# Kernel optimization log

Hardware: AMD Instinct MI355X
Metric: run time of the kernel (lower is better)

The kernel has to match this reference:

```python
import jax, jax.numpy as jnp
import numpy as np
from jax import lax

FILTERS = 256
KERNEL = 1
BATCH, T, D = 16, 2048, 512


def conv1d_same(x, w, b):
    # x: [B, T, Cin], w: [K, Cin, Cout], b: [Cout]
    y = lax.conv_general_dilated(
        x, w, window_strides=(1,), padding='SAME',
        dimension_numbers=('NWC', 'WIO', 'NWC'))
    return y + b


def setup_inputs() -> dict:
    key = jax.random.key(0)
    ks = jax.random.split(key, 5)
    inputs = jax.random.normal(ks[0], (BATCH, T, D), dtype=jnp.float32)
    # Glorot-ish init for conv kernels
    W_qkv = jax.random.normal(ks[1], (KERNEL, D, 3 * FILTERS), dtype=jnp.float32) * (1.0 / np.sqrt(D))
    b_qkv = jnp.zeros((3 * FILTERS,), dtype=jnp.float32)
    W_out = jax.random.normal(ks[2], (KERNEL, FILTERS, D), dtype=jnp.float32) * (1.0 / np.sqrt(FILTERS))
    b_out = jnp.zeros((D,), dtype=jnp.float32)
    return {"inputs": inputs, "W_qkv": W_qkv, "b_qkv": b_qkv, "W_out": W_out, "b_out": b_out}


def reference(inputs, W_qkv, b_qkv, W_out, b_out):
    # QKV projection: conv1d(kernel=1) == pointwise linear, kept general via conv
    qkv = conv1d_same(inputs, W_qkv, b_qkv)          # [B, T, 3F]
    q, k, v = jnp.split(qkv, 3, axis=-1)             # each [B, T, F]
    scale = jnp.sqrt(jnp.asarray(FILTERS, dtype=q.dtype))
    score = jnp.einsum('btf,bsf->bts', q, k) / scale  # [B, T, T]
    attn = jax.nn.softmax(score, axis=-1)
    context = jnp.einsum('bts,bsf->btf', attn, v)    # [B, T, F]
    output = conv1d_same(context, W_out, b_out)      # [B, T, D]
    return inputs + output
```

## Files before the change

### kernel.cpp

```cpp
#include <hip/hip_runtime.h>

typedef __bf16 bf16_t;
typedef __attribute__((ext_vector_type(8))) __bf16 bf16x8;
typedef __attribute__((ext_vector_type(4))) __bf16 bf16x4;
typedef __attribute__((ext_vector_type(4))) float f32x4;

#define GLL16(gsrc, ldst)                                                                   \
  __builtin_amdgcn_global_load_lds(                                                         \
      (const __attribute__((address_space(1))) unsigned int*)(gsrc),                        \
      (__attribute__((address_space(3))) unsigned int*)(ldst), 16, 0, 0)

#define BATCH 16
#define TT    2048
#define DD    512
#define FF    256
#define MTOT  (BATCH * TT)

__global__ __launch_bounds__(256) void cast_all_kernel(const float* __restrict__ x,
                                                       bf16_t* __restrict__ xb,
                                                       const float* __restrict__ Wqkv,
                                                       const float* __restrict__ Wout,
                                                       bf16_t* __restrict__ WqkvT,
                                                       bf16_t* __restrict__ WoutT) {
  const int t0 = blockIdx.x * blockDim.x + threadIdx.x;
  const int stride = gridDim.x * blockDim.x;
  const int n4 = (MTOT * DD) / 4;
  for (int i = t0; i < n4; i += stride) {
    float4 v = ((const float4*)x)[i];
    bf16x4 o;
    o[0] = (bf16_t)v.x; o[1] = (bf16_t)v.y; o[2] = (bf16_t)v.z; o[3] = (bf16_t)v.w;
    ((bf16x4*)xb)[i] = o;
  }
  for (int i = t0; i < 768 * 512 + 512 * 256; i += stride) {
    if (i < 768 * 512) {
      int n = i >> 9, k = i & 511;
      WqkvT[i] = (bf16_t)Wqkv[k * 768 + n];
    } else {
      int i2 = i - 768 * 512;
      int n = i2 >> 8, k = i2 & 255;
      WoutT[i2] = (bf16_t)Wout[k * 512 + n];
    }
  }
}

__global__ __launch_bounds__(256) void gemm_qkv_kernel(const bf16_t* __restrict__ A,
                                                       const bf16_t* __restrict__ Bt,
                                                       const float* __restrict__ bias,
                                                       bf16_t* __restrict__ Qo,
                                                       bf16_t* __restrict__ Ko,
                                                       bf16_t* __restrict__ Vt) {
  __shared__ __align__(16) bf16_t Al[2][128 * 32];
  __shared__ __align__(16) bf16_t Bl[2][128 * 32];
  const int tid = threadIdx.x;
  const int l = tid & 63, w = tid >> 6;
  const int g = l >> 4, r = l & 15;
  const int wm = w >> 1, wn = w & 1;
  const int lin = blockIdx.x;
  const int wid = (lin & 7) * 192 + (lin >> 3);
  const int m0 = (wid / 6) * 128;
  const int n0 = (wid % 6) * 128;
  const int lda = 512, ldb = 512;
  const bf16_t* Abase = A + (size_t)m0 * lda;
  const bf16_t* Bbase = Bt + (size_t)n0 * ldb;

  f32x4 acc[4][4] = {};

  auto stage = [&](int kt, int bufi) {
    const int k0 = kt * 32;
#pragma unroll
    for (int rnd = 0; rnd < 2; ++rnd) {
      int idx = rnd * 256 + tid;
      int row = idx >> 2, d = idx & 3;
      int sc = d ^ ((row >> 1) & 3);
      GLL16(Abase + row * lda + k0 + sc * 8, &Al[bufi][idx * 8]);
    }
#pragma unroll
    for (int rnd = 0; rnd < 2; ++rnd) {
      int idx = rnd * 256 + tid;
      int row = idx >> 2, d = idx & 3;
      int sc = d ^ ((row >> 1) & 3);
      GLL16(Bbase + row * ldb + k0 + sc * 8, &Bl[bufi][idx * 8]);
    }
  };

  stage(0, 0);
  __syncthreads();
  int buf = 0;
  const int NK = 512 / 32;
  for (int kt = 0; kt < NK; ++kt) {
    if (kt + 1 < NK) stage(kt + 1, buf ^ 1);
    bf16x8 af[4], bfr[4];
#pragma unroll
    for (int mi = 0; mi < 4; ++mi) {
      int row = wm * 64 + mi * 16 + r;
      int cc = g ^ ((row >> 1) & 3);
      af[mi] = *(const bf16x8*)&Al[buf][row * 32 + cc * 8];
    }
#pragma unroll
    for (int ni = 0; ni < 4; ++ni) {
      int row = wn * 64 + ni * 16 + r;
      int cc = g ^ ((row >> 1) & 3);
      bfr[ni] = *(const bf16x8*)&Bl[buf][row * 32 + cc * 8];
    }
#pragma unroll
    for (int mi = 0; mi < 4; ++mi)
#pragma unroll
      for (int ni = 0; ni < 4; ++ni)
        acc[mi][ni] = __builtin_amdgcn_mfma_f32_16x16x32_bf16(af[mi], bfr[ni], acc[mi][ni], 0, 0, 0);
    __syncthreads();
    buf ^= 1;
  }

  const int qsel = n0 >> 8;
#pragma unroll
  for (int mi = 0; mi < 4; ++mi) {
    int row0 = m0 + wm * 64 + mi * 16 + g * 4;
#pragma unroll
    for (int ni = 0; ni < 4; ++ni) {
      int col = n0 + wn * 64 + ni * 16 + r;
      float bv = bias[col];
      int cl = col & 255;
      if (qsel == 2) {
        bf16x4 pk;
#pragma unroll
        for (int i = 0; i < 4; ++i) pk[i] = (bf16_t)(acc[mi][ni][i] + bv);
        int b = row0 >> 11, t0 = row0 & 2047;
        *(bf16x4*)&Vt[((size_t)(b * 256 + cl)) * 2048 + t0] = pk;
      } else {
        bf16_t* dst = (qsel == 0) ? Qo : Ko;
#pragma unroll
        for (int i = 0; i < 4; ++i)
          dst[(size_t)(row0 + i) * 256 + cl] = (bf16_t)(acc[mi][ni][i] + bv);
      }
    }
  }
}

__global__ __launch_bounds__(256, 2) void attn_kernel(const bf16_t* __restrict__ Q,
                                                      const bf16_t* __restrict__ K,
                                                      const bf16_t* __restrict__ Vt,
                                                      bf16_t* __restrict__ ctx) {
  __shared__ __align__(16) bf16_t Kl[2][32 * 256];
  __shared__ __align__(16) bf16_t Vl[2][256 * 32];
  __shared__ __align__(16) bf16_t Pl[4][16 * 32];
  const int tid = threadIdx.x;
  const int l = tid & 63, w = tid >> 6;
  const int g = l >> 4, r = l & 15;
  const int lin = blockIdx.x;
  const int wid = (lin & 7) * 64 + (lin >> 3);
  const int b = wid >> 5;
  const int q0 = (wid & 31) * 64 + w * 16;
  const bf16_t* Kb = K + ((size_t)b * TT) * 256;
  const bf16_t* Vb = Vt + (size_t)b * 256 * TT;

  bf16x8 qf[8];
  const bf16_t* Qrow = Q + ((size_t)(b * TT) + q0 + r) * 256;
#pragma unroll
  for (int kf = 0; kf < 8; ++kf) qf[kf] = *(const bf16x8*)(Qrow + kf * 32 + g * 8);

  f32x4 cacc[16] = {};
  float m_run = -3.0e38f, l_run = 0.0f;

  auto stage = [&](int kv0, int bi) {
#pragma unroll
    for (int rnd = 0; rnd < 4; ++rnd) {
      int idx = rnd * 256 + tid;
      int row = idx >> 5, d = idx & 31;
      int sc = d ^ (row & 7);
      GLL16(Kb + (size_t)(kv0 + row) * 256 + sc * 8, &Kl[bi][idx * 8]);
    }
#pragma unroll
    for (int rnd = 0; rnd < 4; ++rnd) {
      int idx = rnd * 256 + tid;
      int row = idx >> 2, d = idx & 3;
      GLL16(Vb + (size_t)row * TT + kv0 + d * 8, &Vl[bi][idx * 8]);
    }
  };

  stage(0, 0);
  __syncthreads();
  int buf = 0;

  for (int kv0 = 0; kv0 < TT; kv0 += 32) {
    if (kv0 + 32 < TT) stage(kv0 + 32, buf ^ 1);

    f32x4 st[2] = {};
    __builtin_amdgcn_s_setprio(1);
#pragma unroll
    for (int kf = 0; kf < 8; ++kf) {
#pragma unroll
      for (int kvf = 0; kvf < 2; ++kvf) {
        int row = kvf * 16 + r;
        int chunk = (kf * 4 + g) ^ (r & 7);
        bf16x8 kfr = *(const bf16x8*)&Kl[buf][row * 256 + chunk * 8];
        st[kvf] = __builtin_amdgcn_mfma_f32_16x16x32_bf16(kfr, qf[kf], st[kvf], 0, 0, 0);
      }
    }
    __builtin_amdgcn_s_setprio(0);

    float s[2][4];
    float tmax = -3.0e38f;
#pragma unroll
    for (int kvf = 0; kvf < 2; ++kvf)
#pragma unroll
      for (int i = 0; i < 4; ++i) {
        s[kvf][i] = st[kvf][i] * 0.0625f;
        tmax = fmaxf(tmax, s[kvf][i]);
      }
    tmax = fmaxf(tmax, __shfl_xor(tmax, 16));
    tmax = fmaxf(tmax, __shfl_xor(tmax, 32));
    if (!__all(tmax - m_run <= 8.0f)) {
      float mnew = fmaxf(m_run, tmax);
      float alpha = __expf(m_run - mnew);
      l_run *= alpha;
#pragma unroll
      for (int fc = 0; fc < 16; ++fc)
#pragma unroll
        for (int i = 0; i < 4; ++i) cacc[fc][i] *= alpha;
      m_run = mnew;
    }
    float psum = 0.0f;
#pragma unroll
    for (int kvf = 0; kvf < 2; ++kvf) {
      bf16x4 pk;
#pragma unroll
      for (int i = 0; i < 4; ++i) {
        float p = __expf(s[kvf][i] - m_run);
        psum += p;
        pk[i] = (bf16_t)p;
      }
      int eidx = r * 32 + (((kvf * 2 + (g >> 1)) ^ (r & 3)) << 3) + (g & 1) * 4;
      *(bf16x4*)&Pl[w][eidx] = pk;
    }
    psum += __shfl_xor(psum, 16);
    psum += __shfl_xor(psum, 32);
    l_run += psum;

    bf16x8 pf = *(const bf16x8*)&Pl[w][r * 32 + ((g ^ (r & 3)) << 3)];
    __builtin_amdgcn_s_setprio(1);
#pragma unroll
    for (int fc = 0; fc < 16; ++fc) {
      int row = fc * 16 + r;
      bf16x8 vf = *(const bf16x8*)&Vl[buf][row * 32 + g * 8];
      cacc[fc] = __builtin_amdgcn_mfma_f32_16x16x32_bf16(vf, pf, cacc[fc], 0, 0, 0);
    }
    __builtin_amdgcn_s_setprio(0);

    __syncthreads();
    buf ^= 1;
  }

  float inv = 1.0f / l_run;
  bf16_t* crow = ctx + ((size_t)(b * TT) + q0 + r) * 256;
#pragma unroll
  for (int fc = 0; fc < 16; ++fc) {
    bf16x4 pk;
#pragma unroll
    for (int i = 0; i < 4; ++i) pk[i] = (bf16_t)(cacc[fc][i] * inv);
    *(bf16x4*)(crow + fc * 16 + g * 4) = pk;
  }
}

__global__ __launch_bounds__(256) void gemm_out_kernel(const bf16_t* __restrict__ A,
                                                       const bf16_t* __restrict__ Bt,
                                                       const float* __restrict__ bias,
                                                       const float* __restrict__ X,
                                                       float* __restrict__ Out) {
  __shared__ __align__(16) bf16_t Al[2][128 * 32];
  __shared__ __align__(16) bf16_t Bl[2][128 * 32];
  const int tid = threadIdx.x;
  const int l = tid & 63, w = tid >> 6;
  const int g = l >> 4, r = l & 15;
  const int wm = w >> 1, wn = w & 1;
  const int lin = blockIdx.x;
  const int wid = (lin & 7) * 128 + (lin >> 3);
  const int m0 = (wid >> 2) * 128;
  const int n0 = (wid & 3) * 128;
  const int lda = 256, ldb = 256;
  const bf16_t* Abase = A + (size_t)m0 * lda;
  const bf16_t* Bbase = Bt + (size_t)n0 * ldb;

  f32x4 acc[4][4] = {};

  auto stage = [&](int kt, int bufi) {
    const int k0 = kt * 32;
#pragma unroll
    for (int rnd = 0; rnd < 2; ++rnd) {
      int idx = rnd * 256 + tid;
      int row = idx >> 2, d = idx & 3;
      int sc = d ^ ((row >> 1) & 3);
      GLL16(Abase + row * lda + k0 + sc * 8, &Al[bufi][idx * 8]);
    }
#pragma unroll
    for (int rnd = 0; rnd < 2; ++rnd) {
      int idx = rnd * 256 + tid;
      int row = idx >> 2, d = idx & 3;
      int sc = d ^ ((row >> 1) & 3);
      GLL16(Bbase + row * ldb + k0 + sc * 8, &Bl[bufi][idx * 8]);
    }
  };

  stage(0, 0);
  __syncthreads();
  int buf = 0;
  const int NK = 256 / 32;
  for (int kt = 0; kt < NK; ++kt) {
    if (kt + 1 < NK) stage(kt + 1, buf ^ 1);
    bf16x8 af[4], bfr[4];
#pragma unroll
    for (int mi = 0; mi < 4; ++mi) {
      int row = wm * 64 + mi * 16 + r;
      int cc = g ^ ((row >> 1) & 3);
      af[mi] = *(const bf16x8*)&Al[buf][row * 32 + cc * 8];
    }
#pragma unroll
    for (int ni = 0; ni < 4; ++ni) {
      int row = wn * 64 + ni * 16 + r;
      int cc = g ^ ((row >> 1) & 3);
      bfr[ni] = *(const bf16x8*)&Bl[buf][row * 32 + cc * 8];
    }
#pragma unroll
    for (int mi = 0; mi < 4; ++mi)
#pragma unroll
      for (int ni = 0; ni < 4; ++ni)
        acc[mi][ni] = __builtin_amdgcn_mfma_f32_16x16x32_bf16(af[mi], bfr[ni], acc[mi][ni], 0, 0, 0);
    __syncthreads();
    buf ^= 1;
  }

#pragma unroll
  for (int mi = 0; mi < 4; ++mi) {
    int row0 = m0 + wm * 64 + mi * 16 + g * 4;
#pragma unroll
    for (int ni = 0; ni < 4; ++ni) {
      int col = n0 + wn * 64 + ni * 16 + r;
      float bv = bias[col];
#pragma unroll
      for (int i = 0; i < 4; ++i) {
        size_t off = (size_t)(row0 + i) * 512 + col;
        Out[off] = acc[mi][ni][i] + bv + X[off];
      }
    }
  }
}

extern "C" void kernel_launch(void* const* d_in, const int* in_sizes, int n_in,
                              void* d_out, int out_size, void* d_ws, size_t ws_size,
                              hipStream_t stream) {
  const float* X    = (const float*)d_in[0];
  const float* Wqkv = (const float*)d_in[1];
  const float* bqkv = (const float*)d_in[2];
  const float* Wout = (const float*)d_in[3];
  const float* bout = (const float*)d_in[4];
  float* out = (float*)d_out;

  char* ws = (char*)d_ws;
  bf16_t* Xbf   = (bf16_t*)ws;
  bf16_t* ctx   = Xbf;
  bf16_t* WqkvT = (bf16_t*)(ws + 33554432);
  bf16_t* WoutT = (bf16_t*)(ws + 34340864);
  bf16_t* Qb    = (bf16_t*)(ws + 34603008);
  bf16_t* Kb    = (bf16_t*)(ws + 51380224);
  bf16_t* Vt    = (bf16_t*)(ws + 68157440);

  cast_all_kernel<<<2048, 256, 0, stream>>>(X, Xbf, Wqkv, Wout, WqkvT, WoutT);
  gemm_qkv_kernel<<<1536, 256, 0, stream>>>(Xbf, WqkvT, bqkv, Qb, Kb, Vt);
  attn_kernel<<<512, 256, 0, stream>>>(Qb, Kb, Vt, ctx);
  gemm_out_kernel<<<1024, 256, 0, stream>>>(ctx, WoutT, bout, X, out);
}
```

Baseline: 328.2 us.

## Process two query groups per wave to reuse K/V fragments across MFMAs

The attention kernel now runs 2 waves per block, each handling 32 query rows as two 16-row groups. Every K and V fragment read from LDS feeds two MFMAs, halving LDS traffic per MFMA. The V tile in LDS gets a new XOR-swizzled layout, and each thread issues twice as many async copies because the block is smaller. The cost is higher register pressure (doubled accumulators and Q fragments) and only 128 threads per block, which may lower occupancy and latency hiding.

New measurement: 376.5 us. 1.15x slower.

```diff
diff --git a/kernel.cpp b/kernel.cpp
--- a/kernel.cpp
+++ b/kernel.cpp
@@ -136,44 +136,50 @@
   }
 }
 
-__global__ __launch_bounds__(256, 2) void attn_kernel(const bf16_t* __restrict__ Q,
+__global__ __launch_bounds__(128, 2) void attn_kernel(const bf16_t* __restrict__ Q,
                                                       const bf16_t* __restrict__ K,
                                                       const bf16_t* __restrict__ Vt,
                                                       bf16_t* __restrict__ ctx) {
   __shared__ __align__(16) bf16_t Kl[2][32 * 256];
-  __shared__ __align__(16) bf16_t Vl[2][256 * 32];
-  __shared__ __align__(16) bf16_t Pl[4][16 * 32];
+  __shared__ __align__(16) bf16_t Vl[2][128 * 64];
+  __shared__ __align__(16) bf16_t Pl[2][2][16 * 32];
   const int tid = threadIdx.x;
   const int l = tid & 63, w = tid >> 6;
   const int g = l >> 4, r = l & 15;
   const int lin = blockIdx.x;
   const int wid = (lin & 7) * 64 + (lin >> 3);
   const int b = wid >> 5;
-  const int q0 = (wid & 31) * 64 + w * 16;
+  const int q0 = (wid & 31) * 64 + w * 32;
   const bf16_t* Kb = K + ((size_t)b * TT) * 256;
   const bf16_t* Vb = Vt + (size_t)b * 256 * TT;
 
-  bf16x8 qf[8];
-  const bf16_t* Qrow = Q + ((size_t)(b * TT) + q0 + r) * 256;
-#pragma unroll
-  for (int kf = 0; kf < 8; ++kf) qf[kf] = *(const bf16x8*)(Qrow + kf * 32 + g * 8);
-
-  f32x4 cacc[16] = {};
-  float m_run = -3.0e38f, l_run = 0.0f;
+  bf16x8 qf[2][8];
+#pragma unroll
+  for (int qg = 0; qg < 2; ++qg) {
+    const bf16_t* Qrow = Q + ((size_t)(b * TT) + q0 + qg * 16 + r) * 256;
+#pragma unroll
+    for (int kf = 0; kf < 8; ++kf) qf[qg][kf] = *(const bf16x8*)(Qrow + kf * 32 + g * 8);
+  }
+
+  f32x4 cacc[16][2] = {};
+  float m_run[2] = {-3.0e38f, -3.0e38f};
+  float l_run[2] = {0.0f, 0.0f};
 
   auto stage = [&](int kv0, int bi) {
 #pragma unroll
-    for (int rnd = 0; rnd < 4; ++rnd) {
-      int idx = rnd * 256 + tid;
+    for (int rnd = 0; rnd < 8; ++rnd) {
+      int idx = rnd * 128 + tid;
       int row = idx >> 5, d = idx & 31;
       int sc = d ^ (row & 7);
       GLL16(Kb + (size_t)(kv0 + row) * 256 + sc * 8, &Kl[bi][idx * 8]);
     }
 #pragma unroll
-    for (int rnd = 0; rnd < 4; ++rnd) {
-      int idx = rnd * 256 + tid;
-      int row = idx >> 2, d = idx & 3;
-      GLL16(Vb + (size_t)row * TT + kv0 + d * 8, &Vl[bi][idx * 8]);
+    for (int rnd = 0; rnd < 8; ++rnd) {
+      int idx = rnd * 128 + tid;
+      int R = idx >> 3, cd = idx & 7;
+      int c = cd ^ (R & 7);
+      int f = 2 * R + (c >> 2);
+      GLL16(Vb + (size_t)f * TT + kv0 + (c & 3) * 8, &Vl[bi][idx * 8]);
     }
   };
 
@@ -184,7 +190,7 @@
   for (int kv0 = 0; kv0 < TT; kv0 += 32) {
     if (kv0 + 32 < TT) stage(kv0 + 32, buf ^ 1);
 
-    f32x4 st[2] = {};
+    f32x4 st[2][2] = {};
     __builtin_amdgcn_s_setprio(1);
 #pragma unroll
     for (int kf = 0; kf < 8; ++kf) {
@@ -193,56 +199,64 @@
         int row = kvf * 16 + r;
         int chunk = (kf * 4 + g) ^ (r & 7);
         bf16x8 kfr = *(const bf16x8*)&Kl[buf][row * 256 + chunk * 8];
-        st[kvf] = __builtin_amdgcn_mfma_f32_16x16x32_bf16(kfr, qf[kf], st[kvf], 0, 0, 0);
+#pragma unroll
+        for (int qg = 0; qg < 2; ++qg)
+          st[kvf][qg] = __builtin_amdgcn_mfma_f32_16x16x32_bf16(kfr, qf[qg][kf], st[kvf][qg], 0, 0, 0);
       }
     }
     __builtin_amdgcn_s_setprio(0);
 
-    float s[2][4];
-    float tmax = -3.0e38f;
-#pragma unroll
-    for (int kvf = 0; kvf < 2; ++kvf)
-#pragma unroll
-      for (int i = 0; i < 4; ++i) {
-        s[kvf][i] = st[kvf][i] * 0.0625f;
-        tmax = fmaxf(tmax, s[kvf][i]);
-      }
-    tmax = fmaxf(tmax, __shfl_xor(tmax, 16));
-    tmax = fmaxf(tmax, __shfl_xor(tmax, 32));
-    if (!__all(tmax - m_run <= 8.0f)) {
-      float mnew = fmaxf(m_run, tmax);
-      float alpha = __expf(m_run - mnew);
-      l_run *= alpha;
-#pragma unroll
-      for (int fc = 0; fc < 16; ++fc)
-#pragma unroll
-        for (int i = 0; i < 4; ++i) cacc[fc][i] *= alpha;
-      m_run = mnew;
-    }
-    float psum = 0.0f;
-#pragma unroll
-    for (int kvf = 0; kvf < 2; ++kvf) {
-      bf16x4 pk;
-#pragma unroll
-      for (int i = 0; i < 4; ++i) {
-        float p = __expf(s[kvf][i] - m_run);
-        psum += p;
-        pk[i] = (bf16_t)p;
-      }
-      int eidx = r * 32 + (((kvf * 2 + (g >> 1)) ^ (r & 3)) << 3) + (g & 1) * 4;
-      *(bf16x4*)&Pl[w][eidx] = pk;
-    }
-    psum += __shfl_xor(psum, 16);
-    psum += __shfl_xor(psum, 32);
-    l_run += psum;
-
-    bf16x8 pf = *(const bf16x8*)&Pl[w][r * 32 + ((g ^ (r & 3)) << 3)];
+#pragma unroll
+    for (int qg = 0; qg < 2; ++qg) {
+      float s[2][4];
+      float tmax = -3.0e38f;
+#pragma unroll
+      for (int kvf = 0; kvf < 2; ++kvf)
+#pragma unroll
+        for (int i = 0; i < 4; ++i) {
+          s[kvf][i] = st[kvf][qg][i] * 0.0625f;
+          tmax = fmaxf(tmax, s[kvf][i]);
+        }
+      tmax = fmaxf(tmax, __shfl_xor(tmax, 16));
+      tmax = fmaxf(tmax, __shfl_xor(tmax, 32));
+      if (!__all(tmax - m_run[qg] <= 8.0f)) {
+        float mnew = fmaxf(m_run[qg], tmax);
+        float alpha = __expf(m_run[qg] - mnew);
+        l_run[qg] *= alpha;
+#pragma unroll
+        for (int fc = 0; fc < 16; ++fc)
+#pragma unroll
+          for (int i = 0; i < 4; ++i) cacc[fc][qg][i] *= alpha;
+        m_run[qg] = mnew;
+      }
+      float psum = 0.0f;
+#pragma unroll
+      for (int kvf = 0; kvf < 2; ++kvf) {
+        bf16x4 pk;
+#pragma unroll
+        for (int i = 0; i < 4; ++i) {
+          float p = __expf(s[kvf][i] - m_run[qg]);
+          psum += p;
+          pk[i] = (bf16_t)p;
+        }
+        int eidx = r * 32 + (((kvf * 2 + (g >> 1)) ^ (r & 3)) << 3) + (g & 1) * 4;
+        *(bf16x4*)&Pl[w][qg][eidx] = pk;
+      }
+      psum += __shfl_xor(psum, 16);
+      psum += __shfl_xor(psum, 32);
+      l_run[qg] += psum;
+    }
+
+    bf16x8 pf0 = *(const bf16x8*)&Pl[w][0][r * 32 + ((g ^ (r & 3)) << 3)];
+    bf16x8 pf1 = *(const bf16x8*)&Pl[w][1][r * 32 + ((g ^ (r & 3)) << 3)];
     __builtin_amdgcn_s_setprio(1);
 #pragma unroll
     for (int fc = 0; fc < 16; ++fc) {
-      int row = fc * 16 + r;
-      bf16x8 vf = *(const bf16x8*)&Vl[buf][row * 32 + g * 8];
-      cacc[fc] = __builtin_amdgcn_mfma_f32_16x16x32_bf16(vf, pf, cacc[fc], 0, 0, 0);
+      int R = fc * 8 + (r >> 1);
+      int cs = ((r & 1) * 4 + g) ^ ((r >> 1) & 7);
+      bf16x8 vfr = *(const bf16x8*)&Vl[buf][R * 64 + cs * 8];
+      cacc[fc][0] = __builtin_amdgcn_mfma_f32_16x16x32_bf16(vfr, pf0, cacc[fc][0], 0, 0, 0);
+      cacc[fc][1] = __builtin_amdgcn_mfma_f32_16x16x32_bf16(vfr, pf1, cacc[fc][1], 0, 0, 0);
     }
     __builtin_amdgcn_s_setprio(0);
 
@@ -250,14 +264,17 @@
     buf ^= 1;
   }
 
-  float inv = 1.0f / l_run;
-  bf16_t* crow = ctx + ((size_t)(b * TT) + q0 + r) * 256;
-#pragma unroll
-  for (int fc = 0; fc < 16; ++fc) {
-    bf16x4 pk;
-#pragma unroll
-    for (int i = 0; i < 4; ++i) pk[i] = (bf16_t)(cacc[fc][i] * inv);
-    *(bf16x4*)(crow + fc * 16 + g * 4) = pk;
+#pragma unroll
+  for (int qg = 0; qg < 2; ++qg) {
+    float inv = 1.0f / l_run[qg];
+    bf16_t* crow = ctx + ((size_t)(b * TT) + q0 + qg * 16 + r) * 256;
+#pragma unroll
+    for (int fc = 0; fc < 16; ++fc) {
+      bf16x4 pk;
+#pragma unroll
+      for (int i = 0; i < 4; ++i) pk[i] = (bf16_t)(cacc[fc][qg][i] * inv);
+      *(bf16x4*)(crow + fc * 16 + g * 4) = pk;
+    }
   }
 }
 
@@ -365,6 +382,6 @@
 
   cast_all_kernel<<<2048, 256, 0, stream>>>(X, Xbf, Wqkv, Wout, WqkvT, WoutT);
   gemm_qkv_kernel<<<1536, 256, 0, stream>>>(Xbf, WqkvT, bqkv, Qb, Kb, Vt);
-  attn_kernel<<<512, 256, 0, stream>>>(Qb, Kb, Vt, ctx);
+  attn_kernel<<<512, 128, 0, stream>>>(Qb, Kb, Vt, ctx);
   gemm_out_kernel<<<1024, 256, 0, stream>>>(ctx, WoutT, bout, X, out);
 }
```

## Split KV in attention, switch to 32x32 MFMA, add merge kernel

Applied to the files above, without the earlier changes.

Attention now splits each batch's KV range into two halves, so each block covers 128 query rows over 1024 keys and writes partial context plus max/sum statistics. A new merge kernel combines the two partials. The inner loops move from 16x16x32 to 32x32x16 MFMA, and P is kept in registers via permlane32 swaps instead of a round trip through LDS, with V swizzled in LDS. The aim is more reuse per K/V tile and less LDS traffic for P. The cost is extra global traffic for the partial contexts and one more kernel launch.

Result: no change. 322.1 us (-1.9%).

```diff
diff --git a/kernel.cpp b/kernel.cpp
--- a/kernel.cpp
+++ b/kernel.cpp
@@ -4,17 +4,27 @@
 typedef __attribute__((ext_vector_type(8))) __bf16 bf16x8;
 typedef __attribute__((ext_vector_type(4))) __bf16 bf16x4;
 typedef __attribute__((ext_vector_type(4))) float f32x4;
+typedef __attribute__((ext_vector_type(16))) float f32x16;
+typedef __attribute__((ext_vector_type(4))) unsigned u32x4;
 
 #define GLL16(gsrc, ldst)                                                                   \
   __builtin_amdgcn_global_load_lds(                                                         \
       (const __attribute__((address_space(1))) unsigned int*)(gsrc),                        \
       (__attribute__((address_space(3))) unsigned int*)(ldst), 16, 0, 0)
+
+#define SWAP32(x, y) asm("v_permlane32_swap_b32 %0, %1" : "+v"(x), "+v"(y))
 
 #define BATCH 16
 #define TT    2048
 #define DD    512
 #define FF    256
 #define MTOT  (BATCH * TT)
+
+static __device__ __forceinline__ unsigned pk2(float a, float b) {
+  unsigned short ua = __builtin_bit_cast(unsigned short, (bf16_t)a);
+  unsigned short ub = __builtin_bit_cast(unsigned short, (bf16_t)b);
+  return (unsigned)ua | ((unsigned)ub << 16);
+}
 
 __global__ __launch_bounds__(256) void cast_all_kernel(const float* __restrict__ x,
                                                        bf16_t* __restrict__ xb,
@@ -139,26 +149,29 @@
 __global__ __launch_bounds__(256, 2) void attn_kernel(const bf16_t* __restrict__ Q,
                                                       const bf16_t* __restrict__ K,
                                                       const bf16_t* __restrict__ Vt,
-                                                      bf16_t* __restrict__ ctx) {
+                                                      bf16_t* __restrict__ ctxp,
+                                                      float2* __restrict__ ml) {
   __shared__ __align__(16) bf16_t Kl[2][32 * 256];
   __shared__ __align__(16) bf16_t Vl[2][256 * 32];
-  __shared__ __align__(16) bf16_t Pl[4][16 * 32];
   const int tid = threadIdx.x;
   const int l = tid & 63, w = tid >> 6;
-  const int g = l >> 4, r = l & 15;
+  const int hi = l >> 5, q31 = l & 31;
   const int lin = blockIdx.x;
   const int wid = (lin & 7) * 64 + (lin >> 3);
   const int b = wid >> 5;
-  const int q0 = (wid & 31) * 64 + w * 16;
+  const int qblk = wid & 15;
+  const int s = (wid >> 4) & 1;
+  const int q0 = qblk * 128 + w * 32;
+  const int kvbase = s * 1024;
   const bf16_t* Kb = K + ((size_t)b * TT) * 256;
   const bf16_t* Vb = Vt + (size_t)b * 256 * TT;
 
-  bf16x8 qf[8];
-  const bf16_t* Qrow = Q + ((size_t)(b * TT) + q0 + r) * 256;
-#pragma unroll
-  for (int kf = 0; kf < 8; ++kf) qf[kf] = *(const bf16x8*)(Qrow + kf * 32 + g * 8);
-
-  f32x4 cacc[16] = {};
+  bf16x8 qf[16];
+  const bf16_t* Qrow = Q + ((size_t)(b * TT) + q0 + q31) * 256;
+#pragma unroll
+  for (int kf = 0; kf < 16; ++kf) qf[kf] = *(const bf16x8*)(Qrow + kf * 16 + hi * 8);
+
+  f32x16 cacc[8] = {};
   float m_run = -3.0e38f, l_run = 0.0f;
 
   auto stage = [&](int kv0, int bi) {
@@ -172,77 +185,75 @@
 #pragma unroll
     for (int rnd = 0; rnd < 4; ++rnd) {
       int idx = rnd * 256 + tid;
-      int row = idx >> 2, d = idx & 3;
-      GLL16(Vb + (size_t)row * TT + kv0 + d * 8, &Vl[bi][idx * 8]);
+      int R = idx >> 2, d = idx & 3;
+      int c = d ^ (R & 3);
+      GLL16(Vb + (size_t)R * TT + kv0 + c * 8, &Vl[bi][idx * 8]);
     }
   };
 
-  stage(0, 0);
+  stage(kvbase, 0);
   __syncthreads();
   int buf = 0;
 
-  for (int kv0 = 0; kv0 < TT; kv0 += 32) {
-    if (kv0 + 32 < TT) stage(kv0 + 32, buf ^ 1);
-
-    f32x4 st[2] = {};
+  for (int t = 0; t < 32; ++t) {
+    const int kv0 = kvbase + t * 32;
+    if (t + 1 < 32) stage(kv0 + 32, buf ^ 1);
+
+    f32x16 st = {};
     __builtin_amdgcn_s_setprio(1);
 #pragma unroll
-    for (int kf = 0; kf < 8; ++kf) {
-#pragma unroll
-      for (int kvf = 0; kvf < 2; ++kvf) {
-        int row = kvf * 16 + r;
-        int chunk = (kf * 4 + g) ^ (r & 7);
-        bf16x8 kfr = *(const bf16x8*)&Kl[buf][row * 256 + chunk * 8];
-        st[kvf] = __builtin_amdgcn_mfma_f32_16x16x32_bf16(kfr, qf[kf], st[kvf], 0, 0, 0);
-      }
+    for (int kf = 0; kf < 16; ++kf) {
+      int chunk = (2 * kf + hi) ^ (q31 & 7);
+      bf16x8 kfr = *(const bf16x8*)&Kl[buf][q31 * 256 + chunk * 8];
+      st = __builtin_amdgcn_mfma_f32_32x32x16_bf16(kfr, qf[kf], st, 0, 0, 0);
     }
     __builtin_amdgcn_s_setprio(0);
 
-    float s[2][4];
     float tmax = -3.0e38f;
 #pragma unroll
-    for (int kvf = 0; kvf < 2; ++kvf)
-#pragma unroll
-      for (int i = 0; i < 4; ++i) {
-        s[kvf][i] = st[kvf][i] * 0.0625f;
-        tmax = fmaxf(tmax, s[kvf][i]);
-      }
-    tmax = fmaxf(tmax, __shfl_xor(tmax, 16));
+    for (int i = 0; i < 16; ++i) tmax = fmaxf(tmax, st[i] * 0.0625f);
     tmax = fmaxf(tmax, __shfl_xor(tmax, 32));
     if (!__all(tmax - m_run <= 8.0f)) {
       float mnew = fmaxf(m_run, tmax);
       float alpha = __expf(m_run - mnew);
       l_run *= alpha;
 #pragma unroll
-      for (int fc = 0; fc < 16; ++fc)
-#pragma unroll
-        for (int i = 0; i < 4; ++i) cacc[fc][i] *= alpha;
+      for (int fc = 0; fc < 8; ++fc)
+#pragma unroll
+        for (int i = 0; i < 16; ++i) cacc[fc][i] *= alpha;
       m_run = mnew;
     }
     float psum = 0.0f;
-#pragma unroll
-    for (int kvf = 0; kvf < 2; ++kvf) {
-      bf16x4 pk;
-#pragma unroll
-      for (int i = 0; i < 4; ++i) {
-        float p = __expf(s[kvf][i] - m_run);
-        psum += p;
-        pk[i] = (bf16_t)p;
-      }
-      int eidx = r * 32 + (((kvf * 2 + (g >> 1)) ^ (r & 3)) << 3) + (g & 1) * 4;
-      *(bf16x4*)&Pl[w][eidx] = pk;
-    }
-    psum += __shfl_xor(psum, 16);
+    float p[16];
+#pragma unroll
+    for (int i = 0; i < 16; ++i) {
+      p[i] = __expf(st[i] * 0.0625f - m_run);
+      psum += p[i];
+    }
     psum += __shfl_xor(psum, 32);
     l_run += psum;
 
-    bf16x8 pf = *(const bf16x8*)&Pl[w][r * 32 + ((g ^ (r & 3)) << 3)];
+    unsigned u00 = pk2(p[0], p[1]),  u01 = pk2(p[2], p[3]);
+    unsigned u10 = pk2(p[4], p[5]),  u11 = pk2(p[6], p[7]);
+    unsigned u20 = pk2(p[8], p[9]),  u21 = pk2(p[10], p[11]);
+    unsigned u30 = pk2(p[12], p[13]), u31 = pk2(p[14], p[15]);
+    SWAP32(u00, u10);
+    SWAP32(u01, u11);
+    SWAP32(u20, u30);
+    SWAP32(u21, u31);
+    u32x4 w0 = {u00, u01, u10, u11};
+    u32x4 w1 = {u20, u21, u30, u31};
+    bf16x8 pf0 = __builtin_bit_cast(bf16x8, w0);
+    bf16x8 pf1 = __builtin_bit_cast(bf16x8, w1);
+
     __builtin_amdgcn_s_setprio(1);
 #pragma unroll
-    for (int fc = 0; fc < 16; ++fc) {
-      int row = fc * 16 + r;
-      bf16x8 vf = *(const bf16x8*)&Vl[buf][row * 32 + g * 8];
-      cacc[fc] = __builtin_amdgcn_mfma_f32_16x16x32_bf16(vf, pf, cacc[fc], 0, 0, 0);
+    for (int fc = 0; fc < 8; ++fc) {
+      int R = fc * 32 + q31;
+      bf16x8 vf0 = *(const bf16x8*)&Vl[buf][R * 32 + ((hi ^ (R & 3)) * 8)];
+      bf16x8 vf1 = *(const bf16x8*)&Vl[buf][R * 32 + (((2 + hi) ^ (R & 3)) * 8)];
+      cacc[fc] = __builtin_amdgcn_mfma_f32_32x32x16_bf16(vf0, pf0, cacc[fc], 0, 0, 0);
+      cacc[fc] = __builtin_amdgcn_mfma_f32_32x32x16_bf16(vf1, pf1, cacc[fc], 0, 0, 0);
     }
     __builtin_amdgcn_s_setprio(0);
 
@@ -251,14 +262,44 @@
   }
 
   float inv = 1.0f / l_run;
-  bf16_t* crow = ctx + ((size_t)(b * TT) + q0 + r) * 256;
-#pragma unroll
-  for (int fc = 0; fc < 16; ++fc) {
-    bf16x4 pk;
-#pragma unroll
-    for (int i = 0; i < 4; ++i) pk[i] = (bf16_t)(cacc[fc][i] * inv);
-    *(bf16x4*)(crow + fc * 16 + g * 4) = pk;
-  }
+  bf16_t* crow = ctxp + (size_t)s * (MTOT * 256) + ((size_t)(b * TT) + q0 + q31) * 256;
+#pragma unroll
+  for (int fc = 0; fc < 8; ++fc) {
+#pragma unroll
+    for (int qd = 0; qd < 4; ++qd) {
+      bf16x4 o;
+#pragma unroll
+      for (int i = 0; i < 4; ++i) o[i] = (bf16_t)(cacc[fc][4 * qd + i] * inv);
+      *(bf16x4*)(crow + fc * 32 + 8 * qd + 4 * hi) = o;
+    }
+  }
+  if (l < 32) {
+    float2 v; v.x = m_run; v.y = l_run;
+    ml[s * MTOT + b * TT + q0 + l] = v;
+  }
+}
+
+__global__ __launch_bounds__(256) void merge_kernel(const bf16_t* __restrict__ c0,
+                                                    const bf16_t* __restrict__ c1,
+                                                    const float2* __restrict__ ml,
+                                                    bf16_t* __restrict__ out) {
+  int t = blockIdx.x * 256 + threadIdx.x;
+  int row = t >> 6;
+  int fo = (t & 63) * 4;
+  float2 a = ml[row];
+  float2 bm = ml[MTOT + row];
+  float M = fmaxf(a.x, bm.x);
+  float w0 = a.y * __expf(a.x - M);
+  float w1 = bm.y * __expf(bm.x - M);
+  float inv = 1.0f / (w0 + w1);
+  w0 *= inv; w1 *= inv;
+  size_t off = (size_t)row * 256 + fo;
+  bf16x4 v0 = *(const bf16x4*)(c0 + off);
+  bf16x4 v1 = *(const bf16x4*)(c1 + off);
+  bf16x4 o;
+#pragma unroll
+  for (int i = 0; i < 4; ++i) o[i] = (bf16_t)((float)v0[i] * w0 + (float)v1[i] * w1);
+  *(bf16x4*)(out + off) = o;
 }
 
 __global__ __launch_bounds__(256) void gemm_out_kernel(const bf16_t* __restrict__ A,
@@ -356,15 +397,20 @@
 
   char* ws = (char*)d_ws;
   bf16_t* Xbf   = (bf16_t*)ws;
-  bf16_t* ctx   = Xbf;
+  bf16_t* ctx0  = (bf16_t*)ws;
+  bf16_t* ctx1  = (bf16_t*)(ws + 16777216);
   bf16_t* WqkvT = (bf16_t*)(ws + 33554432);
   bf16_t* WoutT = (bf16_t*)(ws + 34340864);
   bf16_t* Qb    = (bf16_t*)(ws + 34603008);
   bf16_t* Kb    = (bf16_t*)(ws + 51380224);
   bf16_t* Vt    = (bf16_t*)(ws + 68157440);
+  float2* ml    = (float2*)(ws + 84934656);
+
+  bf16_t* ctxF  = Vt;
 
   cast_all_kernel<<<2048, 256, 0, stream>>>(X, Xbf, Wqkv, Wout, WqkvT, WoutT);
   gemm_qkv_kernel<<<1536, 256, 0, stream>>>(Xbf, WqkvT, bqkv, Qb, Kb, Vt);
-  attn_kernel<<<512, 256, 0, stream>>>(Qb, Kb, Vt, ctx);
-  gemm_out_kernel<<<1024, 256, 0, stream>>>(ctx, WoutT, bout, X, out);
-}
+  attn_kernel<<<512, 256, 0, stream>>>(Qb, Kb, Vt, ctx0, ml);
+  merge_kernel<<<8192, 256, 0, stream>>>(ctx0, ctx1, ml, ctxF);
+  gemm_out_kernel<<<1024, 256, 0, stream>>>(ctxF, WoutT, bout, X, out);
+}
```
